# Kernel tuning notes

Measured on AMD Instinct MI355X. Metric: run time of the kernel, lower is better.

## Reference

```python
import jax, jax.numpy as jnp
import numpy as np

B, S, H = 128, 512, 256
STEP = 1


def setup_inputs() -> dict:
    key = jax.random.key(0)
    ks = jax.random.split(key, 16)
    stdv = 1.0 / np.sqrt(H)
    u = lambda k, shape: jax.random.uniform(k, shape, jnp.float32, -stdv, stdv)
    return {
        "A": jax.random.uniform(ks[0], (B, S, 2 * S), jnp.float32),
        "hidden": jax.random.normal(ks[1], (B, S, H), jnp.float32),
        "mask": jnp.ones((B, S), jnp.int32),
        # linear_edge_in / linear_edge_out (Linear(H, H, bias=True))
        "W_in": u(ks[2], (H, H)),  "b_in": u(ks[3], (H,)),
        "W_out": u(ks[4], (H, H)), "b_out": u(ks[5], (H,)),
        # adjacency biases
        "b_iah": u(ks[6], (H,)), "b_oah": u(ks[7], (H,)),
        # GRU-style gate weights: w_ih [3H, 2H], w_hh [3H, H]
        "w_ih": u(ks[8], (3 * H, 2 * H)), "b_ih": u(ks[9], (3 * H,)),
        "w_hh": u(ks[10], (3 * H, H)),    "b_hh": u(ks[11], (3 * H,)),
    }


def _gnn_cell(A, hidden, W_in, b_in, W_out, b_out, b_iah, b_oah,
              w_ih, b_ih, w_hh, b_hh):
    s = hidden.shape[1]
    # edge-transformed features (torch F.linear: x @ W.T + b)
    h_in = jnp.einsum('bsh,gh->bsg', hidden, W_in) + b_in
    h_out = jnp.einsum('bsh,gh->bsg', hidden, W_out) + b_out
    # adjacency message passing: [B,S,S] @ [B,S,H]
    input_in = jnp.einsum('bij,bjh->bih', A[:, :, :s], h_in) + b_iah
    input_out = jnp.einsum('bij,bjh->bih', A[:, :, s:2 * s], h_out) + b_oah
    inputs = jnp.concatenate([input_in, input_out], axis=2)  # [B,S,2H]
    gi = jnp.einsum('bsi,gi->bsg', inputs, w_ih) + b_ih      # [B,S,3H]
    gh = jnp.einsum('bsh,gh->bsg', hidden, w_hh) + b_hh      # [B,S,3H]
    i_r, i_i, i_n = jnp.split(gi, 3, axis=2)
    h_r, h_i, h_n = jnp.split(gh, 3, axis=2)
    resetgate = jax.nn.sigmoid(i_r + h_r)
    inputgate = jax.nn.sigmoid(i_i + h_i)
    newgate = jnp.tanh(i_n + resetgate * h_n)
    return hidden + inputgate * (newgate - hidden)


def reference(A, hidden, mask, W_in, b_in, W_out, b_out, b_iah, b_oah,
              w_ih, b_ih, w_hh, b_hh):
    # GNN.forward with issrgnn=True: run GNNCell `step` times (mask unused)
    for _ in range(STEP):
        hidden = _gnn_cell(A, hidden, W_in, b_in, W_out, b_out,
                           b_iah, b_oah, w_ih, b_ih, w_hh, b_hh)
    return hidden
```

## Files before the change

### kernel.cpp

```cpp
#include <hip/hip_runtime.h>

#define B_ 128
#define S_ 512
#define H_ 256
#define M_ (B_*S_)

typedef __attribute__((ext_vector_type(4))) float f32x4;
typedef __attribute__((ext_vector_type(8))) short s16x8;
typedef __attribute__((ext_vector_type(4))) unsigned short u16x4;
typedef unsigned short ushort_t;

typedef __attribute__((address_space(1))) void as1_void;
typedef __attribute__((address_space(3))) void as3_void;

__device__ __forceinline__ unsigned short f2h(float f) {
  _Float16 h = (_Float16)f;
  return __builtin_bit_cast(unsigned short, h);
}

__device__ __forceinline__ f32x4 mfma16(s16x8 a, s16x8 b, f32x4 c) {
  asm("v_mfma_f32_16x16x32_f16 %0, %1, %2, %0" : "+v"(c) : "v"(a), "v"(b));
  return c;
}

__device__ __forceinline__ void cp16(const void* g, void* l) {
  __builtin_amdgcn_global_load_lds((as1_void*)g, (as3_void*)l, 16, 0, 0);
}

__device__ __forceinline__ int stage_kc(int lane) {
  return (lane & 3) ^ ((lane >> 3) & 3);
}
__device__ __forceinline__ int frag_off(int s, int lane) {
  int ln = lane & 15, kg = lane >> 4;
  return s * 512 + (ln * 4 + (kg ^ ((ln >> 1) & 3))) * 8;
}

__global__ void k_cvt_f16(const float* __restrict__ in, ushort_t* __restrict__ out, int n8) {
  int i = blockIdx.x * blockDim.x + threadIdx.x;
  if (i >= n8) return;
  const float* p = in + (size_t)i * 8;
  f32x4 a = *(const f32x4*)p;
  f32x4 b = *(const f32x4*)(p + 4);
  s16x8 o;
  o[0]=(short)f2h(a[0]); o[1]=(short)f2h(a[1]); o[2]=(short)f2h(a[2]); o[3]=(short)f2h(a[3]);
  o[4]=(short)f2h(b[0]); o[5]=(short)f2h(b[1]); o[6]=(short)f2h(b[2]); o[7]=(short)f2h(b[3]);
  *(s16x8*)(out + (size_t)i * 8) = o;
}

__global__ __launch_bounds__(256, 2)
void k_gemm1(const ushort_t* __restrict__ hid, const ushort_t* __restrict__ wcat,
             const float* __restrict__ b_in, const float* __restrict__ b_out,
             ushort_t* __restrict__ hcatT) {
  __shared__ __attribute__((aligned(16))) ushort_t lA[2][8*512];
  __shared__ __attribute__((aligned(16))) ushort_t lB[2][16*512];
  const int bb = blockIdx.y;
  const int j0 = (blockIdx.x >> 1) * 128;
  const int n0 = (blockIdx.x & 1) * 256;
  const int tid = threadIdx.x;
  const int w = tid >> 6, lane = tid & 63;
  const int ln = lane & 15, kg = lane >> 4;
  const int wm = w >> 1, wn = w & 1;
  const int srow = lane >> 2, skc = stage_kc(lane);

  f32x4 acc[4][8];
  #pragma unroll
  for (int i = 0; i < 4; ++i)
    #pragma unroll
    for (int j = 0; j < 8; ++j) acc[i][j] = (f32x4){0.f,0.f,0.f,0.f};

  const size_t arow0 = (size_t)bb * 512 + j0;

  auto stage = [&](int t, int bsel) {
    int k0 = t * 32;
    #pragma unroll
    for (int it = 0; it < 2; ++it) {
      int s = it*4 + w;
      cp16(hid + (arow0 + s*16 + srow)*256 + k0 + skc*8, &lA[bsel][s*512]);
    }
    #pragma unroll
    for (int it = 0; it < 4; ++it) {
      int s = it*4 + w;
      cp16(wcat + (size_t)(n0 + s*16 + srow)*256 + k0 + skc*8, &lB[bsel][s*512]);
    }
  };

  stage(0, 0);
  __syncthreads();
  for (int t = 0; t < 8; ++t) {
    int bsel = t & 1;
    if (t + 1 < 8) stage(t + 1, bsel ^ 1);
    s16x8 af[4];
    #pragma unroll
    for (int mf = 0; mf < 4; ++mf)
      af[mf] = *(const s16x8*)&lA[bsel][frag_off(wm*4 + mf, lane)];
    #pragma unroll
    for (int nf = 0; nf < 8; ++nf) {
      s16x8 bf = *(const s16x8*)&lB[bsel][frag_off(wn*8 + nf, lane)];
      #pragma unroll
      for (int mf = 0; mf < 4; ++mf) acc[mf][nf] = mfma16(af[mf], bf, acc[mf][nf]);
    }
    __syncthreads();
  }

  #pragma unroll
  for (int nf = 0; nf < 8; ++nf) {
    int gn = n0 + wn*128 + nf*16 + ln;
    float bias = (gn < 256) ? b_in[gn] : b_out[gn - 256];
    #pragma unroll
    for (int mf = 0; mf < 4; ++mf) {
      int j = j0 + wm*64 + mf*16 + kg*4;
      u16x4 v;
      #pragma unroll
      for (int r = 0; r < 4; ++r) v[r] = f2h(acc[mf][nf][r] + bias);
      *(u16x4*)&hcatT[((size_t)(bb*512 + gn))*512 + j] = v;
    }
  }
}

__global__ __launch_bounds__(256, 2)
void k_gemm2(const float* __restrict__ A, const ushort_t* __restrict__ hcatT,
             const float* __restrict__ b_iah, const float* __restrict__ b_oah,
             ushort_t* __restrict__ inp) {
  __shared__ __attribute__((aligned(16))) ushort_t lA[2][8*512];
  __shared__ __attribute__((aligned(16))) ushort_t lB[2][16*512];
  const int bb = blockIdx.y;
  const int i0 = (blockIdx.x >> 1) * 128;
  const int half = blockIdx.x & 1;
  const int n0 = half * 256;
  const int tid = threadIdx.x;
  const int w = tid >> 6, lane = tid & 63;
  const int ln = lane & 15, kg = lane >> 4;
  const int wm = w >> 1, wn = w & 1;
  const int srow = lane >> 2, skc = stage_kc(lane);

  f32x4 acc[4][8];
  #pragma unroll
  for (int i = 0; i < 4; ++i)
    #pragma unroll
    for (int j = 0; j < 8; ++j) acc[i][j] = (f32x4){0.f,0.f,0.f,0.f};

  const float* Abase = A + ((size_t)bb*512 + i0)*1024 + half*512;

  auto loadA = [&](int t, f32x4* ra) {
    int k0 = t * 32;
    #pragma unroll
    for (int it = 0; it < 2; ++it) {
      int s = it*4 + w;
      const float* p = Abase + (size_t)(s*16 + srow)*1024 + k0 + skc*8;
      ra[it*2]   = *(const f32x4*)p;
      ra[it*2+1] = *(const f32x4*)(p + 4);
    }
  };
  auto stageB = [&](int t, int bsel) {
    int k0 = t * 32;
    #pragma unroll
    for (int it = 0; it < 4; ++it) {
      int s = it*4 + w;
      cp16(hcatT + ((size_t)(bb*512 + n0 + s*16 + srow))*512 + k0 + skc*8, &lB[bsel][s*512]);
    }
  };
  auto writeA = [&](const f32x4* ra, int bsel) {
    #pragma unroll
    for (int it = 0; it < 2; ++it) {
      int s = it*4 + w;
      s16x8 o;
      o[0]=(short)f2h(ra[it*2][0]); o[1]=(short)f2h(ra[it*2][1]);
      o[2]=(short)f2h(ra[it*2][2]); o[3]=(short)f2h(ra[it*2][3]);
      o[4]=(short)f2h(ra[it*2+1][0]); o[5]=(short)f2h(ra[it*2+1][1]);
      o[6]=(short)f2h(ra[it*2+1][2]); o[7]=(short)f2h(ra[it*2+1][3]);
      *(s16x8*)&lA[bsel][s*512 + lane*8] = o;
    }
  };

  { f32x4 ra[4]; loadA(0, ra); stageB(0, 0); writeA(ra, 0); }
  __syncthreads();
  for (int t = 0; t < 16; ++t) {
    int bsel = t & 1;
    f32x4 ra[4];
    if (t + 1 < 16) { loadA(t + 1, ra); stageB(t + 1, bsel ^ 1); }
    s16x8 af[4];
    #pragma unroll
    for (int mf = 0; mf < 4; ++mf)
      af[mf] = *(const s16x8*)&lA[bsel][frag_off(wm*4 + mf, lane)];
    #pragma unroll
    for (int nf = 0; nf < 8; ++nf) {
      s16x8 bf = *(const s16x8*)&lB[bsel][frag_off(wn*8 + nf, lane)];
      #pragma unroll
      for (int mf = 0; mf < 4; ++mf) acc[mf][nf] = mfma16(af[mf], bf, acc[mf][nf]);
    }
    if (t + 1 < 16) writeA(ra, bsel ^ 1);
    __syncthreads();
  }

  #pragma unroll
  for (int nf = 0; nf < 8; ++nf) {
    int gn = n0 + wn*128 + nf*16 + ln;
    float bias = half ? b_oah[gn - 256] : b_iah[gn];
    #pragma unroll
    for (int mf = 0; mf < 4; ++mf) {
      #pragma unroll
      for (int r = 0; r < 4; ++r) {
        int i = i0 + wm*64 + mf*16 + kg*4 + r;
        inp[((size_t)(bb*512 + i))*512 + gn] = f2h(acc[mf][nf][r] + bias);
      }
    }
  }
}

__global__ __launch_bounds__(256, 2)
void k_gemm3(const ushort_t* __restrict__ inp, const ushort_t* __restrict__ hidh,
             const ushort_t* __restrict__ wih, const ushort_t* __restrict__ whh,
             const float* __restrict__ b_ih, const float* __restrict__ b_hh,
             const float* __restrict__ hidden, float* __restrict__ out) {
  __shared__ __attribute__((aligned(16))) ushort_t lIn[3][8*512];
  __shared__ __attribute__((aligned(16))) ushort_t lW[3][12*512];
  const int m0 = blockIdx.y * 128;
  const int h0 = blockIdx.x * 64;
  const int tid = threadIdx.x;
  const int w = tid >> 6, lane = tid & 63;
  const int ln = lane & 15, kg = lane >> 4;
  const int srow = lane >> 2, skc = stage_kc(lane);

  f32x4 aR[2][4], aI[2][4], aIN[2][4], aHN[2][4];
  #pragma unroll
  for (int m = 0; m < 2; ++m)
    #pragma unroll
    for (int n = 0; n < 4; ++n) {
      aR[m][n] = (f32x4){0.f,0.f,0.f,0.f}; aI[m][n] = (f32x4){0.f,0.f,0.f,0.f};
      aIN[m][n] = (f32x4){0.f,0.f,0.f,0.f}; aHN[m][n] = (f32x4){0.f,0.f,0.f,0.f};
    }

  auto stage = [&](int gs, int bsel) {
    if (gs < 16) {
      int k0 = gs * 32;
      #pragma unroll
      for (int it = 0; it < 2; ++it) {
        int s = it*4 + w;
        cp16(inp + (size_t)(m0 + s*16 + srow)*512 + k0 + skc*8, &lIn[bsel][s*512]);
      }
      #pragma unroll
      for (int it = 0; it < 3; ++it) {
        int s = it*4 + w;
        int row = s*16 + srow, g = row >> 6, r = row & 63;
        cp16(wih + (size_t)(g*256 + h0 + r)*512 + k0 + skc*8, &lW[bsel][s*512]);
      }
    } else {
      int k0 = (gs - 16) * 32;
      #pragma unroll
      for (int it = 0; it < 2; ++it) {
        int s = it*4 + w;
        cp16(hidh + (size_t)(m0 + s*16 + srow)*256 + k0 + skc*8, &lIn[bsel][s*512]);
      }
      #pragma unroll
      for (int it = 0; it < 3; ++it) {
        int s = it*4 + w;
        int row = s*16 + srow, g = row >> 6, r = row & 63;
        cp16(whh + (size_t)(g*256 + h0 + r)*256 + k0 + skc*8, &lW[bsel][s*512]);
      }
    }
  };

  auto compute = [&](int cur, f32x4 (&aN)[2][4]) {
    s16x8 af[2];
    #pragma unroll
    for (int mf = 0; mf < 2; ++mf)
      af[mf] = *(const s16x8*)&lIn[cur][frag_off(w*2 + mf, lane)];
    #pragma unroll
    for (int g = 0; g < 3; ++g) {
      #pragma unroll
      for (int nf = 0; nf < 4; ++nf) {
        s16x8 bf = *(const s16x8*)&lW[cur][frag_off(g*4 + nf, lane)];
        #pragma unroll
        for (int mf = 0; mf < 2; ++mf) {
          f32x4& a = (g == 0 ? aR[mf][nf] : g == 1 ? aI[mf][nf] : aN[mf][nf]);
          a = mfma16(af[mf], bf, a);
        }
      }
    }
  };

  stage(0, 0);
  stage(1, 1);
  for (int t = 0; t < 16; ++t) {
    int cur = t % 3;
    asm volatile("s_waitcnt vmcnt(5)" ::: "memory");
    __builtin_amdgcn_s_barrier();
    stage(t + 2, (t + 2) % 3);
    compute(cur, aIN);
  }
  for (int t = 16; t < 23; ++t) {
    int cur = t % 3;
    asm volatile("s_waitcnt vmcnt(5)" ::: "memory");
    __builtin_amdgcn_s_barrier();
    if (t + 2 < 24) stage(t + 2, (t + 2) % 3);
    compute(cur, aHN);
  }
  {
    asm volatile("s_waitcnt vmcnt(0)" ::: "memory");
    __builtin_amdgcn_s_barrier();
    compute(23 % 3, aHN);
  }

  #pragma unroll
  for (int nf = 0; nf < 4; ++nf) {
    int h = h0 + nf*16 + ln;
    float br  = b_ih[h]       + b_hh[h];
    float bi  = b_ih[256 + h] + b_hh[256 + h];
    float bni = b_ih[512 + h];
    float bnh = b_hh[512 + h];
    #pragma unroll
    for (int mf = 0; mf < 2; ++mf) {
      #pragma unroll
      for (int r = 0; r < 4; ++r) {
        int m = m0 + w*32 + mf*16 + kg*4 + r;
        float rg = 1.0f / (1.0f + __expf(-(aR[mf][nf][r] + br)));
        float ig = 1.0f / (1.0f + __expf(-(aI[mf][nf][r] + bi)));
        float narg = aIN[mf][nf][r] + bni + rg * (aHN[mf][nf][r] + bnh);
        float e2 = __expf(2.0f * narg);
        float ng = 1.0f - 2.0f / (e2 + 1.0f);
        float hv = hidden[(size_t)m*256 + h];
        out[(size_t)m*256 + h] = hv + ig * (ng - hv);
      }
    }
  }
}

extern "C" void kernel_launch(void* const* d_in, const int* in_sizes, int n_in,
                              void* d_out, int out_size, void* d_ws, size_t ws_size,
                              hipStream_t stream) {
  const float* A      = (const float*)d_in[0];
  const float* hidden = (const float*)d_in[1];
  const float* W_in   = (const float*)d_in[3];
  const float* b_in   = (const float*)d_in[4];
  const float* W_out  = (const float*)d_in[5];
  const float* b_out  = (const float*)d_in[6];
  const float* b_iah  = (const float*)d_in[7];
  const float* b_oah  = (const float*)d_in[8];
  const float* w_ih   = (const float*)d_in[9];
  const float* b_ih   = (const float*)d_in[10];
  const float* w_hh   = (const float*)d_in[11];
  const float* b_hh   = (const float*)d_in[12];
  float* out = (float*)d_out;

  char* ws = (char*)d_ws;
  ushort_t* hidh  = (ushort_t*)(ws);
  ushort_t* wcat  = (ushort_t*)(ws + 33554432);
  ushort_t* wihh  = (ushort_t*)(ws + 33816576);
  ushort_t* whhh  = (ushort_t*)(ws + 34603008);
  ushort_t* hcatT = (ushort_t*)(ws + 34996224);
  ushort_t* inp   = (ushort_t*)(ws + 102105088);

  k_cvt_f16<<<8192, 256, 0, stream>>>(hidden, hidh, M_*H_/8);
  k_cvt_f16<<<32,   256, 0, stream>>>(W_in,  wcat,           H_*H_/8);
  k_cvt_f16<<<32,   256, 0, stream>>>(W_out, wcat + H_*H_,   H_*H_/8);
  k_cvt_f16<<<192,  256, 0, stream>>>(w_ih,  wihh, 768*512/8);
  k_cvt_f16<<<96,   256, 0, stream>>>(w_hh,  whhh, 768*256/8);

  k_gemm1<<<dim3(8, 128), 256, 0, stream>>>(hidh, wcat, b_in, b_out, hcatT);
  k_gemm2<<<dim3(8, 128), 256, 0, stream>>>(A, hcatT, b_iah, b_oah, inp);
  k_gemm3<<<dim3(4, 512), 256, 0, stream>>>(inp, hidh, wihh, whhh, b_ih, b_hh, hidden, out);
}
```

Baseline: 299.4 us.

## Triple-buffer GEMM pipelines, remap block order, rebalance gemm3 warp tiling, add setprio

In gemm1 and gemm2, the double-buffered loads separated by __syncthreads are replaced with a three-stage cp16 pipeline governed by explicit vmcnt waits and raw barriers. gemm2 also keeps two register sets of A prefetch in flight. All three GEMMs remap the flat block index so that consecutive blocks are spread across the grid, which appears aimed at XCD/L2 locality. Their MFMA sections are wrapped in s_setprio. gemm3 switches its warp tiling from 2x4 to 4x2 fragments per warp to increase A-fragment reuse. The trade-off is higher LDS use in gemm1/gemm2, which may reduce occupancy, and the vmcnt accounting has to be exactly right.

```diff
diff --git a/kernel.cpp b/kernel.cpp
--- a/kernel.cpp
+++ b/kernel.cpp
@@ -25,6 +25,17 @@
 
 __device__ __forceinline__ void cp16(const void* g, void* l) {
   __builtin_amdgcn_global_load_lds((as1_void*)g, (as3_void*)l, 16, 0, 0);
+}
+
+__device__ __forceinline__ void waitvm(int n) {
+  switch (n) {
+    case 0:  asm volatile("s_waitcnt vmcnt(0)"  ::: "memory"); break;
+    case 4:  asm volatile("s_waitcnt vmcnt(4)"  ::: "memory"); break;
+    case 5:  asm volatile("s_waitcnt vmcnt(5)"  ::: "memory"); break;
+    case 6:  asm volatile("s_waitcnt vmcnt(6)"  ::: "memory"); break;
+    case 8:  asm volatile("s_waitcnt vmcnt(8)"  ::: "memory"); break;
+    case 12: asm volatile("s_waitcnt vmcnt(12)" ::: "memory"); break;
+  }
 }
 
 __device__ __forceinline__ int stage_kc(int lane) {
@@ -51,11 +62,13 @@
 void k_gemm1(const ushort_t* __restrict__ hid, const ushort_t* __restrict__ wcat,
              const float* __restrict__ b_in, const float* __restrict__ b_out,
              ushort_t* __restrict__ hcatT) {
-  __shared__ __attribute__((aligned(16))) ushort_t lA[2][8*512];
-  __shared__ __attribute__((aligned(16))) ushort_t lB[2][16*512];
-  const int bb = blockIdx.y;
-  const int j0 = (blockIdx.x >> 1) * 128;
-  const int n0 = (blockIdx.x & 1) * 256;
+  __shared__ __attribute__((aligned(16))) ushort_t lA[3][8*512];
+  __shared__ __attribute__((aligned(16))) ushort_t lB[3][16*512];
+  const int flat = blockIdx.y * 8 + blockIdx.x;
+  const int orig = (flat & 7) * 128 + (flat >> 3);
+  const int bx = orig & 7, bb = orig >> 3;
+  const int j0 = (bx >> 1) * 128;
+  const int n0 = (bx & 1) * 256;
   const int tid = threadIdx.x;
   const int w = tid >> 6, lane = tid & 63;
   const int ln = lane & 15, kg = lane >> 4;
@@ -83,24 +96,30 @@
       cp16(wcat + (size_t)(n0 + s*16 + srow)*256 + k0 + skc*8, &lB[bsel][s*512]);
     }
   };
-
-  stage(0, 0);
-  __syncthreads();
-  for (int t = 0; t < 8; ++t) {
-    int bsel = t & 1;
-    if (t + 1 < 8) stage(t + 1, bsel ^ 1);
+  auto compute = [&](int cur) {
     s16x8 af[4];
     #pragma unroll
     for (int mf = 0; mf < 4; ++mf)
-      af[mf] = *(const s16x8*)&lA[bsel][frag_off(wm*4 + mf, lane)];
+      af[mf] = *(const s16x8*)&lA[cur][frag_off(wm*4 + mf, lane)];
+    __builtin_amdgcn_s_setprio(1);
     #pragma unroll
     for (int nf = 0; nf < 8; ++nf) {
-      s16x8 bf = *(const s16x8*)&lB[bsel][frag_off(wn*8 + nf, lane)];
+      s16x8 bf = *(const s16x8*)&lB[cur][frag_off(wn*8 + nf, lane)];
       #pragma unroll
       for (int mf = 0; mf < 4; ++mf) acc[mf][nf] = mfma16(af[mf], bf, acc[mf][nf]);
     }
-    __syncthreads();
-  }
+    __builtin_amdgcn_s_setprio(0);
+  };
+
+  stage(0, 0); stage(1, 1);
+  for (int t = 0; t < 6; ++t) {
+    waitvm(6);
+    __builtin_amdgcn_s_barrier();
+    stage(t + 2, (t + 2) % 3);
+    compute(t % 3);
+  }
+  waitvm(6); __builtin_amdgcn_s_barrier(); compute(6 % 3);
+  waitvm(0); __builtin_amdgcn_s_barrier(); compute(7 % 3);
 
   #pragma unroll
   for (int nf = 0; nf < 8; ++nf) {
@@ -122,10 +141,12 @@
              const float* __restrict__ b_iah, const float* __restrict__ b_oah,
              ushort_t* __restrict__ inp) {
   __shared__ __attribute__((aligned(16))) ushort_t lA[2][8*512];
-  __shared__ __attribute__((aligned(16))) ushort_t lB[2][16*512];
-  const int bb = blockIdx.y;
-  const int i0 = (blockIdx.x >> 1) * 128;
-  const int half = blockIdx.x & 1;
+  __shared__ __attribute__((aligned(16))) ushort_t lB[3][16*512];
+  const int flat = blockIdx.y * 8 + blockIdx.x;
+  const int orig = (flat & 7) * 128 + (flat >> 3);
+  const int bx = orig & 7, bb = orig >> 3;
+  const int i0 = (bx >> 1) * 128;
+  const int half = bx & 1;
   const int n0 = half * 256;
   const int tid = threadIdx.x;
   const int w = tid >> 6, lane = tid & 63;
@@ -140,15 +161,16 @@
     for (int j = 0; j < 8; ++j) acc[i][j] = (f32x4){0.f,0.f,0.f,0.f};
 
   const float* Abase = A + ((size_t)bb*512 + i0)*1024 + half*512;
-
-  auto loadA = [&](int t, f32x4* ra) {
+  f32x4 ra[2][4];
+
+  auto loadA = [&](int t, f32x4 (&r)[4]) {
     int k0 = t * 32;
     #pragma unroll
     for (int it = 0; it < 2; ++it) {
       int s = it*4 + w;
       const float* p = Abase + (size_t)(s*16 + srow)*1024 + k0 + skc*8;
-      ra[it*2]   = *(const f32x4*)p;
-      ra[it*2+1] = *(const f32x4*)(p + 4);
+      r[it*2]   = *(const f32x4*)p;
+      r[it*2+1] = *(const f32x4*)(p + 4);
     }
   };
   auto stageB = [&](int t, int bsel) {
@@ -159,37 +181,50 @@
       cp16(hcatT + ((size_t)(bb*512 + n0 + s*16 + srow))*512 + k0 + skc*8, &lB[bsel][s*512]);
     }
   };
-  auto writeA = [&](const f32x4* ra, int bsel) {
+  auto writeA = [&](const f32x4 (&r)[4], int bsel) {
     #pragma unroll
     for (int it = 0; it < 2; ++it) {
       int s = it*4 + w;
       s16x8 o;
-      o[0]=(short)f2h(ra[it*2][0]); o[1]=(short)f2h(ra[it*2][1]);
-      o[2]=(short)f2h(ra[it*2][2]); o[3]=(short)f2h(ra[it*2][3]);
-      o[4]=(short)f2h(ra[it*2+1][0]); o[5]=(short)f2h(ra[it*2+1][1]);
-      o[6]=(short)f2h(ra[it*2+1][2]); o[7]=(short)f2h(ra[it*2+1][3]);
+      o[0]=(short)f2h(r[it*2][0]); o[1]=(short)f2h(r[it*2][1]);
+      o[2]=(short)f2h(r[it*2][2]); o[3]=(short)f2h(r[it*2][3]);
+      o[4]=(short)f2h(r[it*2+1][0]); o[5]=(short)f2h(r[it*2+1][1]);
+      o[6]=(short)f2h(r[it*2+1][2]); o[7]=(short)f2h(r[it*2+1][3]);
       *(s16x8*)&lA[bsel][s*512 + lane*8] = o;
     }
   };
-
-  { f32x4 ra[4]; loadA(0, ra); stageB(0, 0); writeA(ra, 0); }
-  __syncthreads();
+  auto compute = [&](int acur, int bcur) {
+    s16x8 af[4];
+    #pragma unroll
+    for (int mf = 0; mf < 4; ++mf)
+      af[mf] = *(const s16x8*)&lA[acur][frag_off(wm*4 + mf, lane)];
+    __builtin_amdgcn_s_setprio(1);
+    #pragma unroll
+    for (int nf = 0; nf < 8; ++nf) {
+      s16x8 bf = *(const s16x8*)&lB[bcur][frag_off(wn*8 + nf, lane)];
+      #pragma unroll
+      for (int mf = 0; mf < 4; ++mf) acc[mf][nf] = mfma16(af[mf], bf, acc[mf][nf]);
+    }
+    __builtin_amdgcn_s_setprio(0);
+  };
+
+  loadA(0, ra[0]); stageB(0, 0);
+  loadA(1, ra[1]); stageB(1, 1);
+  waitvm(12);
+  writeA(ra[0], 0);
+  asm volatile("s_waitcnt lgkmcnt(0)" ::: "memory");
+
+  #pragma unroll
   for (int t = 0; t < 16; ++t) {
-    int bsel = t & 1;
-    f32x4 ra[4];
-    if (t + 1 < 16) { loadA(t + 1, ra); stageB(t + 1, bsel ^ 1); }
-    s16x8 af[4];
-    #pragma unroll
-    for (int mf = 0; mf < 4; ++mf)
-      af[mf] = *(const s16x8*)&lA[bsel][frag_off(wm*4 + mf, lane)];
-    #pragma unroll
-    for (int nf = 0; nf < 8; ++nf) {
-      s16x8 bf = *(const s16x8*)&lB[bsel][frag_off(wn*8 + nf, lane)];
-      #pragma unroll
-      for (int mf = 0; mf < 4; ++mf) acc[mf][nf] = mfma16(af[mf], bf, acc[mf][nf]);
-    }
-    if (t + 1 < 16) writeA(ra, bsel ^ 1);
-    __syncthreads();
+    waitvm(t < 15 ? 8 : 0);
+    __builtin_amdgcn_s_barrier();
+    if (t + 2 < 16) { loadA(t + 2, ra[t & 1]); stageB(t + 2, (t + 2) % 3); }
+    compute(t & 1, t % 3);
+    if (t + 1 < 16) {
+      waitvm(t + 2 < 16 ? 12 : 4);
+      writeA(ra[(t + 1) & 1], (t + 1) & 1);
+      asm volatile("s_waitcnt lgkmcnt(0)" ::: "memory");
+    }
   }
 
   #pragma unroll
@@ -214,18 +249,21 @@
              const float* __restrict__ hidden, float* __restrict__ out) {
   __shared__ __attribute__((aligned(16))) ushort_t lIn[3][8*512];
   __shared__ __attribute__((aligned(16))) ushort_t lW[3][12*512];
-  const int m0 = blockIdx.y * 128;
-  const int h0 = blockIdx.x * 64;
+  const int flat = blockIdx.y * 4 + blockIdx.x;
+  const int orig = (flat & 7) * 256 + (flat >> 3);
+  const int h0 = (orig & 3) * 64;
+  const int m0 = (orig >> 2) * 128;
   const int tid = threadIdx.x;
   const int w = tid >> 6, lane = tid & 63;
   const int ln = lane & 15, kg = lane >> 4;
+  const int wm2 = w >> 1, wh = w & 1;
   const int srow = lane >> 2, skc = stage_kc(lane);
 
-  f32x4 aR[2][4], aI[2][4], aIN[2][4], aHN[2][4];
-  #pragma unroll
-  for (int m = 0; m < 2; ++m)
-    #pragma unroll
-    for (int n = 0; n < 4; ++n) {
+  f32x4 aR[4][2], aI[4][2], aIN[4][2], aHN[4][2];
+  #pragma unroll
+  for (int m = 0; m < 4; ++m)
+    #pragma unroll
+    for (int n = 0; n < 2; ++n) {
       aR[m][n] = (f32x4){0.f,0.f,0.f,0.f}; aI[m][n] = (f32x4){0.f,0.f,0.f,0.f};
       aIN[m][n] = (f32x4){0.f,0.f,0.f,0.f}; aHN[m][n] = (f32x4){0.f,0.f,0.f,0.f};
     }
@@ -260,59 +298,56 @@
     }
   };
 
-  auto compute = [&](int cur, f32x4 (&aN)[2][4]) {
-    s16x8 af[2];
-    #pragma unroll
-    for (int mf = 0; mf < 2; ++mf)
-      af[mf] = *(const s16x8*)&lIn[cur][frag_off(w*2 + mf, lane)];
+  auto compute = [&](int cur, f32x4 (&aN)[4][2]) {
+    s16x8 af[4];
+    #pragma unroll
+    for (int mf = 0; mf < 4; ++mf)
+      af[mf] = *(const s16x8*)&lIn[cur][frag_off(wm2*4 + mf, lane)];
+    __builtin_amdgcn_s_setprio(1);
     #pragma unroll
     for (int g = 0; g < 3; ++g) {
       #pragma unroll
-      for (int nf = 0; nf < 4; ++nf) {
-        s16x8 bf = *(const s16x8*)&lW[cur][frag_off(g*4 + nf, lane)];
+      for (int nf = 0; nf < 2; ++nf) {
+        s16x8 bf = *(const s16x8*)&lW[cur][frag_off(g*4 + wh*2 + nf, lane)];
         #pragma unroll
-        for (int mf = 0; mf < 2; ++mf) {
+        for (int mf = 0; mf < 4; ++mf) {
           f32x4& a = (g == 0 ? aR[mf][nf] : g == 1 ? aI[mf][nf] : aN[mf][nf]);
           a = mfma16(af[mf], bf, a);
         }
       }
     }
+    __builtin_amdgcn_s_setprio(0);
   };
 
   stage(0, 0);
   stage(1, 1);
   for (int t = 0; t < 16; ++t) {
-    int cur = t % 3;
-    asm volatile("s_waitcnt vmcnt(5)" ::: "memory");
+    waitvm(5);
     __builtin_amdgcn_s_barrier();
     stage(t + 2, (t + 2) % 3);
-    compute(cur, aIN);
-  }
-  for (int t = 16; t < 23; ++t) {
-    int cur = t % 3;
-    asm volatile("s_waitcnt vmcnt(5)" ::: "memory");
+    compute(t % 3, aIN);
+  }
+  for (int t = 16; t < 22; ++t) {
+    waitvm(5);
     __builtin_amdgcn_s_barrier();
-    if (t + 2 < 24) stage(t + 2, (t + 2) % 3);
-    compute(cur, aHN);
-  }
-  {
-    asm volatile("s_waitcnt vmcnt(0)" ::: "memory");
-    __builtin_amdgcn_s_barrier();
-    compute(23 % 3, aHN);
-  }
-
-  #pragma unroll
-  for (int nf = 0; nf < 4; ++nf) {
-    int h = h0 + nf*16 + ln;
+    stage(t + 2, (t + 2) % 3);
+    compute(t % 3, aHN);
+  }
+  waitvm(5); __builtin_amdgcn_s_barrier(); compute(22 % 3, aHN);
+  waitvm(0); __builtin_amdgcn_s_barrier(); compute(23 % 3, aHN);
+
+  #pragma unroll
+  for (int nf = 0; nf < 2; ++nf) {
+    int h = h0 + wh*32 + nf*16 + ln;
     float br  = b_ih[h]       + b_hh[h];
     float bi  = b_ih[256 + h] + b_hh[256 + h];
     float bni = b_ih[512 + h];
     float bnh = b_hh[512 + h];
     #pragma unroll
-    for (int mf = 0; mf < 2; ++mf) {
+    for (int mf = 0; mf < 4; ++mf) {
       #pragma unroll
       for (int r = 0; r < 4; ++r) {
-        int m = m0 + w*32 + mf*16 + kg*4 + r;
+        int m = m0 + wm2*64 + mf*16 + kg*4 + r;
         float rg = 1.0f / (1.0f + __expf(-(aR[mf][nf][r] + br)));
         float ig = 1.0f / (1.0f + __expf(-(aI[mf][nf][r] + bi)));
         float narg = aIN[mf][nf][r] + bni + rg * (aHN[mf][nf][r] + bnh);
```

After: 283.4 us. -5.3%, faster.
